# Performance work log

Measured on AMD Instinct MI355X. Metric: run time of the kernel, lower is better.

## Reference

```python
import jax, jax.numpy as jnp
import numpy as np

BLANK = 127
NEG = -1e30  # effective -inf that stays finite in fp32 arithmetic


def setup_inputs() -> dict:
    key = jax.random.key(0)
    k1, k2 = jax.random.split(key)
    outputs = jax.random.normal(k1, (64, 2048, 128), dtype=jnp.float32)
    # labels in [0, 127) -> never equal to blank (127)
    targets = jax.random.randint(k2, (64, 128), 0, BLANK)
    return {"outputs": outputs, "targets": targets}


def _ctc_loss(outputs, targets):
    # outputs: [B, T, V] logits, targets: [B, S] int labels (no blanks inside)
    B, T, V = outputs.shape
    S = targets.shape[1]
    L = 2 * S + 1  # extended label sequence length (blanks interleaved)

    log_probs = jax.nn.log_softmax(outputs, axis=2)  # [B, T, V]

    # extended labels: blank, y1, blank, y2, ..., blank
    ext = jnp.full((B, L), BLANK, dtype=targets.dtype)
    ext = ext.at[:, 1::2].set(targets)  # [B, L]

    # skip transition (l-2 -> l) allowed iff ext[l] != blank and ext[l] != ext[l-2]
    skip = jnp.concatenate(
        [jnp.zeros((B, 2), dtype=bool),
         (ext[:, 2:] != BLANK) & (ext[:, 2:] != ext[:, :-2])],
        axis=1,
    )  # [B, L]

    # gather per-step log-probs of extended labels: [B, T, L] -> [T, B, L]
    lp_ext = jnp.take_along_axis(log_probs, ext[:, None, :], axis=2)
    lp_ext = jnp.swapaxes(lp_ext, 0, 1)

    # alpha init at t=0: only states 0 (blank) and 1 (first label) reachable
    alpha0 = jnp.full((B, L), NEG, dtype=log_probs.dtype)
    alpha0 = alpha0.at[:, 0].set(lp_ext[0, :, 0])
    alpha0 = alpha0.at[:, 1].set(lp_ext[0, :, 1])

    neg1 = jnp.full((B, 1), NEG, dtype=log_probs.dtype)
    neg2 = jnp.full((B, 2), NEG, dtype=log_probs.dtype)

    def step(alpha, lp):
        s1 = jnp.concatenate([neg1, alpha[:, :-1]], axis=1)
        s2 = jnp.concatenate([neg2, alpha[:, :-2]], axis=1)
        s2 = jnp.where(skip, s2, NEG)
        alpha = lp + jnp.logaddexp(jnp.logaddexp(alpha, s1), s2)
        return alpha, None

    alphaT, _ = jax.lax.scan(step, alpha0, lp_ext[1:])

    # P(targets | outputs) ends in last blank or last label
    loss_b = -jnp.logaddexp(alphaT[:, L - 1], alphaT[:, L - 2])  # [B]

    # zero_infinity=True: unreachable paths -> zero loss
    loss_b = jnp.where(loss_b > 1e29, 0.0, loss_b)

    # reduction='mean': divide each loss by its target length, then batch-mean
    tl = jnp.sum(targets != BLANK, axis=1).astype(loss_b.dtype)
    return jnp.mean(loss_b / jnp.maximum(tl, 1.0))


def reference(outputs, targets):
    return _ctc_loss(outputs, targets)
```

## Files before the change

kernel.cpp:

```cpp
#include <hip/hip_runtime.h>
#include <stdint.h>


#define B_ 64
#define T_ 2048
#define V_ 128
#define S_ 128
#define BLANK 127
#define NCH 512

__global__ __launch_bounds__(256) void lse_kernel(const float* __restrict__ outp,
                                                  float2* __restrict__ lse2) {
  const float L2E = 1.4426950408889634f;
  int gtid = blockIdx.x * 256 + threadIdx.x;
  int wave = gtid >> 6;
  int lane = threadIdx.x & 63;
  long row = (long)wave * 2 + (lane >> 5);
  const float4 x = *(const float4*)(outp + row * V_ + (long)(lane & 31) * 4);
  float ex = exp2f(x.x * L2E), ey = exp2f(x.y * L2E);
  float ez = exp2f(x.z * L2E), ew = exp2f(x.w * L2E);
  float s = (ex + ey) + (ez + ew);
#pragma unroll
  for (int o = 1; o <= 16; o <<= 1) s += __shfl_xor(s, o);
  float bx = __shfl(x.w, (lane < 32) ? 31 : 63);
  if ((lane & 31) == 0) {
    float l2s = log2f(s);
    lse2[row] = make_float2(l2s, exp2f(fmaf(bx, L2E, -l2s)));
  }
}

struct Slot {
  float2 r0, r1, r2, r3;
  float4 la, lb;
};

__global__ __launch_bounds__(64, 1) void ctc_alpha(const float* __restrict__ x,
                                                   const float2* __restrict__ lse2,
                                                   const int* __restrict__ tgt,
                                                   float* __restrict__ lossb) {
  const float L2E = 1.4426950408889634f;
  const int b = blockIdx.x;
  const int k = threadIdx.x;
  const bool kz = (k == 0);

  const int2 tg = ((const int2*)(tgt + b * S_))[k];
  const int t1p = __shfl_up(tg.y, 1);
  const float sk0 = (k > 0 && tg.x != t1p) ? 1.0f : 0.0f;
  const float sk1 = (tg.y != tg.x) ? 1.0f : 0.0f;
  const int tl = __popcll(__ballot(tg.x != BLANK)) + __popcll(__ballot(tg.y != BLANK));
  const int ad0 = (tg.x >> 1) << 2, ad1 = (tg.y >> 1) << 2;
  const bool cs0 = tg.x & 1, cs1 = tg.y & 1;

  const float2* xb2 = (const float2*)(x + (long)b * T_ * V_);
  const float2* lse2b = lse2 + (long)b * T_;

  Slot s0_, s1_, s2_, s3_, s4_, s5_, s6_, s7_;
  float u00, u01, u10, u11, u20, u21, u30, u31, uB0, uB1, uB2, uB3;
  float w00, w01, w10, w11, w20, w21, w30, w31, wB0, wB1, wB2, wB3;
  float a0 = 0.f, a1 = 0.f, a2 = 0.f, a3 = 0.f, a4 = 0.f;
  float adj = kz ? 0.f : 1.0f;
  int P = 0;

#define LOADSLOT(S, CC) do {                                          \
    const float2* rp_ = xb2 + (CC) * 256;                             \
    (S).r0 = rp_[k]; (S).r1 = rp_[64 + k];                            \
    (S).r2 = rp_[128 + k]; (S).r3 = rp_[192 + k];                     \
    const float4* lp_ = (const float4*)(lse2b + (CC) * 4);            \
    (S).la = lp_[0]; (S).lb = lp_[1];                                 \
  } while (0)

#define GS(RR, AD, ODD) ({                                            \
    int h_ = __builtin_amdgcn_ds_bpermute((AD), __float_as_int((RR).x)); \
    int g_ = __builtin_amdgcn_ds_bpermute((AD), __float_as_int((RR).y)); \
    __int_as_float((ODD) ? g_ : h_); })

#define GATHER(S, Q) do {                                             \
    float v_;                                                         \
    v_ = GS((S).r0, ad0, cs0); Q##00 = exp2f(fmaf(v_, L2E, -(S).la.x)); \
    v_ = GS((S).r0, ad1, cs1); Q##01 = exp2f(fmaf(v_, L2E, -(S).la.x)); \
    v_ = GS((S).r1, ad0, cs0); Q##10 = exp2f(fmaf(v_, L2E, -(S).la.z)); \
    v_ = GS((S).r1, ad1, cs1); Q##11 = exp2f(fmaf(v_, L2E, -(S).la.z)); \
    v_ = GS((S).r2, ad0, cs0); Q##20 = exp2f(fmaf(v_, L2E, -(S).lb.x)); \
    v_ = GS((S).r2, ad1, cs1); Q##21 = exp2f(fmaf(v_, L2E, -(S).lb.x)); \
    v_ = GS((S).r3, ad0, cs0); Q##30 = exp2f(fmaf(v_, L2E, -(S).lb.z)); \
    v_ = GS((S).r3, ad1, cs1); Q##31 = exp2f(fmaf(v_, L2E, -(S).lb.z)); \
    Q##B0 = (S).la.y; Q##B1 = (S).la.w;                               \
    Q##B2 = (S).lb.y; Q##B3 = (S).lb.w;                               \
  } while (0)

#define SUBSTEP(P0, P1, PB) do {                                      \
    float s1r = __shfl_up(a3, 1);                                     \
    float s1v = s1r * adj;                                            \
    float na0 = (PB) * (a0 + s1v);                                    \
    float na1 = (P0) * (a1 + fmaf(sk0, s1v, a0));                     \
    float na2 = (PB) * (a2 + a1);                                     \
    float na3 = (P1) * (a3 + fmaf(sk1, a1, a2));                      \
    float na4 = (PB) * (a4 + a3);                                     \
    a0 = na0; a1 = na1; a2 = na2; a3 = na3; a4 = na4;                 \
  } while (0)

#define RESCALE do {                                                  \
    float ml = fmaxf(fmaxf(a0, a1), fmaxf(fmaxf(a2, a3), a4));        \
    int Plo = __shfl_up(P, 1);                                        \
    bool dead = (ml == 0.0f);                                         \
    int e = (int)((__float_as_uint(ml) >> 23) & 255) - 127;           \
    float sc = dead ? 1.0f : __uint_as_float((uint32_t)(127 - e) << 23); \
    a0 *= sc; a1 *= sc; a2 *= sc; a3 *= sc; a4 *= sc;                 \
    P = dead ? Plo : (P + e);                                         \
    int Pl2 = __shfl_up(P, 1);                                        \
    adj = ldexpf(kz ? 0.f : 1.0f, Pl2 - P);                           \
  } while (0)

#define BODY(SJ, SN, CUR, NXT, BASE, JOFF, INIT) do {                 \
    const int c_ = (BASE) + (JOFF);                                   \
    LOADSLOT(SJ, (c_ + 8) & (NCH - 1));                               \
    GATHER(SN, NXT);                                                  \
    if ((INIT) && c_ == 0) {      \
      a0 = kz ? CUR##B0 : 0.f;                                        \
      a1 = kz ? CUR##00 : 0.f;                                        \
    } else {                                                          \
      SUBSTEP(CUR##00, CUR##01, CUR##B0);                             \
    }                                                                 \
    SUBSTEP(CUR##10, CUR##11, CUR##B1);                               \
    SUBSTEP(CUR##20, CUR##21, CUR##B2);                               \
    SUBSTEP(CUR##30, CUR##31, CUR##B3);                               \
    if ((JOFF) & 1) RESCALE;                                          \
    __builtin_amdgcn_sched_barrier(0);                                \
  } while (0)

  LOADSLOT(s0_, 0); LOADSLOT(s1_, 1); LOADSLOT(s2_, 2); LOADSLOT(s3_, 3);
  LOADSLOT(s4_, 4); LOADSLOT(s5_, 5); LOADSLOT(s6_, 6); LOADSLOT(s7_, 7);
  GATHER(s0_, u);
  __builtin_amdgcn_sched_barrier(0);

  for (int blk = 0; blk < NCH / 8; ++blk) {
    const int base = blk << 3;
    BODY(s0_, s1_, u, w, base, 0, 1);
    BODY(s1_, s2_, w, u, base, 1, 0);
    BODY(s2_, s3_, u, w, base, 2, 0);
    BODY(s3_, s4_, w, u, base, 3, 0);
    BODY(s4_, s5_, u, w, base, 4, 0);
    BODY(s5_, s6_, w, u, base, 5, 0);
    BODY(s6_, s7_, u, w, base, 6, 0);
    BODY(s7_, s0_, w, u, base, 7, 0);
  }
#undef BODY
#undef RESCALE
#undef SUBSTEP
#undef GATHER
#undef GS
#undef LOADSLOT

  if (k == 63) {
    float aE = a3 + a4;
    float lb = -(logf(aE) + (float)P * 0.6931471805599453f);
    if (!(lb < 1e29f)) lb = 0.0f;
    lossb[b] = lb / fmaxf((float)tl, 1.0f);
  }
}

__global__ __launch_bounds__(64) void finalize_kernel(const float* __restrict__ lossb,
                                                      float* __restrict__ outv) {
  int k = threadIdx.x;
  float v = lossb[k];
#pragma unroll
  for (int o = 1; o < 64; o <<= 1) v += __shfl_xor(v, o);
  if (k == 0) outv[0] = v * (1.0f / B_);
}

extern "C" void kernel_launch(void* const* d_in, const int* in_sizes, int n_in,
                              void* d_out, int out_size, void* d_ws, size_t ws_size,
                              hipStream_t stream) {
  const float* outputs = (const float*)d_in[0];
  const int* targets = (const int*)d_in[1];
  float2* lse2 = (float2*)d_ws;
  float* lossb = (float*)((char*)d_ws + (size_t)B_ * T_ * sizeof(float2));
  float* outv = (float*)d_out;

  lse_kernel<<<16384, 256, 0, stream>>>(outputs, lse2);
  ctc_alpha<<<B_, 64, 0, stream>>>(outputs, lse2, targets, lossb);
  finalize_kernel<<<1, 64, 0, stream>>>(lossb, outv);
}
```

Before: 387.7 us.

## Issue slot loads via inline asm with partial vmcnt waits and hoisted shuffle

Replaces compiler-generated loads in the alpha recursion with inline-asm global loads that use rolling register offsets, plus an explicit s_waitcnt vmcnt(42). This keeps seven slots of loads in flight instead of letting the compiler insert conservative full waits. The cross-lane shuffle of a3 is also moved to the end of each substep, and redone after rescale, so it is off the critical path of the next step. The hand-counted vmcnt is fragile: if the compiler emits any other memory ops, the wait count is wrong and data may be consumed before it arrives.

```diff
diff --git a/kernel.cpp b/kernel.cpp
--- a/kernel.cpp
+++ b/kernel.cpp
@@ -54,102 +54,124 @@
   const float2* xb2 = (const float2*)(x + (long)b * T_ * V_);
   const float2* lse2b = lse2 + (long)b * T_;
 
+  uint32_t roff = (uint32_t)k * 8u;
+  uint32_t loff = 0u;
+
   Slot s0_, s1_, s2_, s3_, s4_, s5_, s6_, s7_;
   float u00, u01, u10, u11, u20, u21, u30, u31, uB0, uB1, uB2, uB3;
   float w00, w01, w10, w11, w20, w21, w30, w31, wB0, wB1, wB2, wB3;
   float a0 = 0.f, a1 = 0.f, a2 = 0.f, a3 = 0.f, a4 = 0.f;
+  float sh3 = 0.f;
   float adj = kz ? 0.f : 1.0f;
   int P = 0;
 
-#define LOADSLOT(S, CC) do {                                          \
-    const float2* rp_ = xb2 + (CC) * 256;                             \
-    (S).r0 = rp_[k]; (S).r1 = rp_[64 + k];                            \
-    (S).r2 = rp_[128 + k]; (S).r3 = rp_[192 + k];                     \
-    const float4* lp_ = (const float4*)(lse2b + (CC) * 4);            \
-    (S).la = lp_[0]; (S).lb = lp_[1];                                 \
-  } while (0)
-
-#define GS(RR, AD, ODD) ({                                            \
-    int h_ = __builtin_amdgcn_ds_bpermute((AD), __float_as_int((RR).x)); \
-    int g_ = __builtin_amdgcn_ds_bpermute((AD), __float_as_int((RR).y)); \
+#define LOADSLOT(S) do {                                                     \
+    asm volatile("global_load_dwordx2 %0, %1, %2"                            \
+                 : "=v"((S).r0) : "v"(roff), "s"(xb2));                      \
+    asm volatile("global_load_dwordx2 %0, %1, %2 offset:512"                 \
+                 : "=v"((S).r1) : "v"(roff), "s"(xb2));                      \
+    asm volatile("global_load_dwordx2 %0, %1, %2 offset:1024"                \
+                 : "=v"((S).r2) : "v"(roff), "s"(xb2));                      \
+    asm volatile("global_load_dwordx2 %0, %1, %2 offset:1536"                \
+                 : "=v"((S).r3) : "v"(roff), "s"(xb2));                      \
+    asm volatile("global_load_dwordx4 %0, %1, %2"                            \
+                 : "=v"((S).la) : "v"(loff), "s"(lse2b));                    \
+    asm volatile("global_load_dwordx4 %0, %1, %2 offset:16"                  \
+                 : "=v"((S).lb) : "v"(loff), "s"(lse2b));                    \
+    roff = (roff + 2048u) & 0xFFFFFu;                                        \
+    loff = (loff + 32u) & 0x3FFFu;                                           \
+  } while (0)
+
+#define VMWAIT do {                                                          \
+    asm volatile("s_waitcnt vmcnt(42)" ::: "memory");                        \
+    __builtin_amdgcn_sched_barrier(0);                                       \
+  } while (0)
+
+#define GS(RR, AD, ODD) ({                                                   \
+    int h_ = __builtin_amdgcn_ds_bpermute((AD), __float_as_int((RR).x));     \
+    int g_ = __builtin_amdgcn_ds_bpermute((AD), __float_as_int((RR).y));     \
     __int_as_float((ODD) ? g_ : h_); })
 
-#define GATHER(S, Q) do {                                             \
-    float v_;                                                         \
-    v_ = GS((S).r0, ad0, cs0); Q##00 = exp2f(fmaf(v_, L2E, -(S).la.x)); \
-    v_ = GS((S).r0, ad1, cs1); Q##01 = exp2f(fmaf(v_, L2E, -(S).la.x)); \
-    v_ = GS((S).r1, ad0, cs0); Q##10 = exp2f(fmaf(v_, L2E, -(S).la.z)); \
-    v_ = GS((S).r1, ad1, cs1); Q##11 = exp2f(fmaf(v_, L2E, -(S).la.z)); \
-    v_ = GS((S).r2, ad0, cs0); Q##20 = exp2f(fmaf(v_, L2E, -(S).lb.x)); \
-    v_ = GS((S).r2, ad1, cs1); Q##21 = exp2f(fmaf(v_, L2E, -(S).lb.x)); \
-    v_ = GS((S).r3, ad0, cs0); Q##30 = exp2f(fmaf(v_, L2E, -(S).lb.z)); \
-    v_ = GS((S).r3, ad1, cs1); Q##31 = exp2f(fmaf(v_, L2E, -(S).lb.z)); \
-    Q##B0 = (S).la.y; Q##B1 = (S).la.w;                               \
-    Q##B2 = (S).lb.y; Q##B3 = (S).lb.w;                               \
-  } while (0)
-
-#define SUBSTEP(P0, P1, PB) do {                                      \
-    float s1r = __shfl_up(a3, 1);                                     \
-    float s1v = s1r * adj;                                            \
-    float na0 = (PB) * (a0 + s1v);                                    \
-    float na1 = (P0) * (a1 + fmaf(sk0, s1v, a0));                     \
-    float na2 = (PB) * (a2 + a1);                                     \
-    float na3 = (P1) * (a3 + fmaf(sk1, a1, a2));                      \
-    float na4 = (PB) * (a4 + a3);                                     \
-    a0 = na0; a1 = na1; a2 = na2; a3 = na3; a4 = na4;                 \
-  } while (0)
-
-#define RESCALE do {                                                  \
-    float ml = fmaxf(fmaxf(a0, a1), fmaxf(fmaxf(a2, a3), a4));        \
-    int Plo = __shfl_up(P, 1);                                        \
-    bool dead = (ml == 0.0f);                                         \
-    int e = (int)((__float_as_uint(ml) >> 23) & 255) - 127;           \
-    float sc = dead ? 1.0f : __uint_as_float((uint32_t)(127 - e) << 23); \
-    a0 *= sc; a1 *= sc; a2 *= sc; a3 *= sc; a4 *= sc;                 \
-    P = dead ? Plo : (P + e);                                         \
-    int Pl2 = __shfl_up(P, 1);                                        \
-    adj = ldexpf(kz ? 0.f : 1.0f, Pl2 - P);                           \
-  } while (0)
-
-#define BODY(SJ, SN, CUR, NXT, BASE, JOFF, INIT) do {                 \
-    const int c_ = (BASE) + (JOFF);                                   \
-    LOADSLOT(SJ, (c_ + 8) & (NCH - 1));                               \
-    GATHER(SN, NXT);                                                  \
-    if ((INIT) && c_ == 0) {      \
-      a0 = kz ? CUR##B0 : 0.f;                                        \
-      a1 = kz ? CUR##00 : 0.f;                                        \
-    } else {                                                          \
-      SUBSTEP(CUR##00, CUR##01, CUR##B0);                             \
-    }                                                                 \
-    SUBSTEP(CUR##10, CUR##11, CUR##B1);                               \
-    SUBSTEP(CUR##20, CUR##21, CUR##B2);                               \
-    SUBSTEP(CUR##30, CUR##31, CUR##B3);                               \
-    if ((JOFF) & 1) RESCALE;                                          \
-    __builtin_amdgcn_sched_barrier(0);                                \
-  } while (0)
-
-  LOADSLOT(s0_, 0); LOADSLOT(s1_, 1); LOADSLOT(s2_, 2); LOADSLOT(s3_, 3);
-  LOADSLOT(s4_, 4); LOADSLOT(s5_, 5); LOADSLOT(s6_, 6); LOADSLOT(s7_, 7);
+#define GATHER(S, Q) do {                                                    \
+    float v_;                                                                \
+    v_ = GS((S).r0, ad0, cs0); Q##00 = exp2f(fmaf(v_, L2E, -(S).la.x));      \
+    v_ = GS((S).r0, ad1, cs1); Q##01 = exp2f(fmaf(v_, L2E, -(S).la.x));      \
+    v_ = GS((S).r1, ad0, cs0); Q##10 = exp2f(fmaf(v_, L2E, -(S).la.z));      \
+    v_ = GS((S).r1, ad1, cs1); Q##11 = exp2f(fmaf(v_, L2E, -(S).la.z));      \
+    v_ = GS((S).r2, ad0, cs0); Q##20 = exp2f(fmaf(v_, L2E, -(S).lb.x));      \
+    v_ = GS((S).r2, ad1, cs1); Q##21 = exp2f(fmaf(v_, L2E, -(S).lb.x));      \
+    v_ = GS((S).r3, ad0, cs0); Q##30 = exp2f(fmaf(v_, L2E, -(S).lb.z));      \
+    v_ = GS((S).r3, ad1, cs1); Q##31 = exp2f(fmaf(v_, L2E, -(S).lb.z));      \
+    Q##B0 = (S).la.y; Q##B1 = (S).la.w;                                      \
+    Q##B2 = (S).lb.y; Q##B3 = (S).lb.w;                                      \
+  } while (0)
+
+#define SUBSTEP(P0, P1, PB) do {                                             \
+    float s1v = sh3 * adj;                                                   \
+    float na0 = (PB) * (a0 + s1v);                                           \
+    float na1 = (P0) * (a1 + fmaf(sk0, s1v, a0));                            \
+    float na2 = (PB) * (a2 + a1);                                            \
+    float na3 = (P1) * (a3 + fmaf(sk1, a1, a2));                             \
+    float na4 = (PB) * (a4 + a3);                                            \
+    sh3 = __shfl_up(na3, 1);  \
+    a0 = na0; a1 = na1; a2 = na2; a3 = na3; a4 = na4;                        \
+  } while (0)
+
+#define RESCALE do {                                                         \
+    float ml = fmaxf(fmaxf(a0, a1), fmaxf(fmaxf(a2, a3), a4));               \
+    int Plo = __shfl_up(P, 1);                                               \
+    bool dead = (ml == 0.0f);                                                \
+    int e = (int)((__float_as_uint(ml) >> 23) & 255) - 127;                  \
+    float sc = dead ? 1.0f : __uint_as_float((uint32_t)(127 - e) << 23);     \
+    a0 *= sc; a1 *= sc; a2 *= sc; a3 *= sc; a4 *= sc;                        \
+    P = dead ? Plo : (P + e);                                                \
+    int Pl2 = __shfl_up(P, 1);                                               \
+    adj = ldexpf(kz ? 0.f : 1.0f, Pl2 - P);                                  \
+    sh3 = __shfl_up(a3, 1);   \
+  } while (0)
+
+#define BODY(SJ, SN, CUR, NXT, DOINIT, ODD) do {                             \
+    LOADSLOT(SJ);                    \
+    VMWAIT;                       \
+    GATHER(SN, NXT);                          \
+    if (DOINIT) {                        \
+      a0 = kz ? CUR##B0 : 0.f;                                               \
+      a1 = kz ? CUR##00 : 0.f;                                               \
+    } else {                                                                 \
+      SUBSTEP(CUR##00, CUR##01, CUR##B0);                                    \
+    }                                                                        \
+    SUBSTEP(CUR##10, CUR##11, CUR##B1);                                      \
+    SUBSTEP(CUR##20, CUR##21, CUR##B2);                                      \
+    SUBSTEP(CUR##30, CUR##31, CUR##B3);                                      \
+    if (ODD) RESCALE;                                                        \
+    __builtin_amdgcn_sched_barrier(0);                                       \
+  } while (0)
+
+  LOADSLOT(s0_); LOADSLOT(s1_); LOADSLOT(s2_); LOADSLOT(s3_);
+  LOADSLOT(s4_); LOADSLOT(s5_); LOADSLOT(s6_); LOADSLOT(s7_);
+  VMWAIT;
   GATHER(s0_, u);
   __builtin_amdgcn_sched_barrier(0);
 
   for (int blk = 0; blk < NCH / 8; ++blk) {
-    const int base = blk << 3;
-    BODY(s0_, s1_, u, w, base, 0, 1);
-    BODY(s1_, s2_, w, u, base, 1, 0);
-    BODY(s2_, s3_, u, w, base, 2, 0);
-    BODY(s3_, s4_, w, u, base, 3, 0);
-    BODY(s4_, s5_, u, w, base, 4, 0);
-    BODY(s5_, s6_, w, u, base, 5, 0);
-    BODY(s6_, s7_, u, w, base, 6, 0);
-    BODY(s7_, s0_, w, u, base, 7, 0);
+    BODY(s0_, s1_, u, w, (blk == 0), 0);
+    BODY(s1_, s2_, w, u, false, 1);
+    BODY(s2_, s3_, u, w, false, 0);
+    BODY(s3_, s4_, w, u, false, 1);
+    BODY(s4_, s5_, u, w, false, 0);
+    BODY(s5_, s6_, w, u, false, 1);
+    BODY(s6_, s7_, u, w, false, 0);
+    BODY(s7_, s0_, w, u, false, 1);
   }
 #undef BODY
 #undef RESCALE
 #undef SUBSTEP
 #undef GATHER
 #undef GS
+#undef VMWAIT
 #undef LOADSLOT
+
+  asm volatile("s_waitcnt vmcnt(0)" ::: "memory");
 
   if (k == 63) {
     float aE = a3 + a4;
```

After: 350.4 us. 9.6% less time.
